# Optimization experiments

Measured on AMD Instinct MI355X. Metric: run time of the kernel, lower is better.

## Reference

```python
import jax, jax.numpy as jnp
import numpy as np

DK = 64  # embedding_size / h = 1024 / 16


def setup_inputs() -> dict:
    key = jax.random.key(0)
    k1, k2, k3 = jax.random.split(key, 3)
    S = 8192
    return {
        "q": jax.random.normal(k1, (S, DK), dtype=jnp.float32),
        "k": jax.random.normal(k2, (S, DK), dtype=jnp.float32),
        "v": jax.random.normal(k3, (S, DK), dtype=jnp.float32),
    }


def reference(q, k, v):
    # scores: [S, S]; NOTE: source scales by 1/dk (not 1/sqrt(dk)) — kept faithful.
    qk = jnp.matmul(q, k.T) * (1.0 / DK)
    S = qk.shape[0]
    # causal mask: position (i, j) allowed iff i >= j (0 added), else -inf
    i = jnp.arange(S)[:, None]
    j = jnp.arange(S)[None, :]
    qk = jnp.where(i >= j, qk, -jnp.inf)
    attn = jax.nn.softmax(qk, axis=-1)
    return jnp.matmul(attn, v)
```

## Files before the change

kernel.cpp:

```cpp
#include <hip/hip_runtime.h>
#include <hip/hip_bf16.h>

#define S_LEN 8192
#define DKD   64
#define BM    64
#define BN    64
#define PAD   8
#define LDK   (DKD + PAD)

#define CHUNK 1024
#define NC    (S_LEN / CHUNK)

#define WS_NEED ((size_t)2 * S_LEN * DKD * 2 + (size_t)NC * S_LEN * 4 + (size_t)NC * S_LEN * DKD * 2)

typedef __bf16 bf16x8 __attribute__((ext_vector_type(8)));
typedef float  f32x4  __attribute__((ext_vector_type(4)));
typedef unsigned short ushort8v __attribute__((ext_vector_type(8)));
typedef unsigned short ushort4v __attribute__((ext_vector_type(4)));

__device__ __forceinline__ unsigned short f2bf(float f) {
  union { float f; unsigned u; } v; v.f = f;
  unsigned u = v.u;
  return (unsigned short)((u + 0x7fffu + ((u >> 16) & 1u)) >> 16);
}
__device__ __forceinline__ float bf2f(unsigned short s) {
  union { unsigned u; float f; } v; v.u = ((unsigned)s) << 16;
  return v.f;
}
__device__ __forceinline__ unsigned pk2(float a, float b) {
  union { float f; unsigned u; } x, y; x.f = a; y.f = b;
  return ((x.u + 0x8000u) >> 16) | ((y.u + 0x8000u) & 0xffff0000u);
}
__device__ __forceinline__ bf16x8 q_frag8(const float* p, float sc) {
  float4 u = *(const float4*)p;
  float4 w = *(const float4*)(p + 4);
  union { ushort8v s; bf16x8 b; } r;
  r.s[0] = f2bf(u.x * sc); r.s[1] = f2bf(u.y * sc);
  r.s[2] = f2bf(u.z * sc); r.s[3] = f2bf(u.w * sc);
  r.s[4] = f2bf(w.x * sc); r.s[5] = f2bf(w.y * sc);
  r.s[6] = f2bf(w.z * sc); r.s[7] = f2bf(w.w * sc);
  return r.b;
}

__global__ __launch_bounds__(256) void precompute(const float* __restrict__ k,
                                                  const float* __restrict__ v,
                                                  unsigned short* __restrict__ Kb,
                                                  unsigned short* __restrict__ Vtb) {
  __shared__ unsigned short Ls[64][72];
  const int b = blockIdx.x, tid = threadIdx.x;
  if (blockIdx.y == 0) {
    size_t base = (size_t)b * 64 * DKD;
#pragma unroll
    for (int j = 0; j < 4; ++j) {
      int vi = tid + j * 256;
      float4 x = *(const float4*)(k + base + (size_t)vi * 4);
      ushort4v o = { f2bf(x.x), f2bf(x.y), f2bf(x.z), f2bf(x.w) };
      *(ushort4v*)(Kb + base + (size_t)vi * 4) = o;
    }
  } else {
#pragma unroll
    for (int j = 0; j < 4; ++j) {
      int vi = tid + j * 256;
      int row = vi >> 4, c4 = vi & 15;
      float4 x = *(const float4*)(v + ((size_t)(b * 64 + row)) * DKD + c4 * 4);
      Ls[row][c4 * 4 + 0] = f2bf(x.x);
      Ls[row][c4 * 4 + 1] = f2bf(x.y);
      Ls[row][c4 * 4 + 2] = f2bf(x.z);
      Ls[row][c4 * 4 + 3] = f2bf(x.w);
    }
    __syncthreads();
#pragma unroll
    for (int j = 0; j < 4; ++j) {
      int ci = tid + j * 256;
      int d = ci >> 4, c0 = ci & 15;
      ushort4v o = { Ls[c0][d], Ls[c0 + 16][d], Ls[c0 + 32][d], Ls[c0 + 48][d] };
      *(ushort4v*)(Vtb + (size_t)d * S_LEN + b * 64 + c0 * 4) = o;
    }
  }
}

__global__ __launch_bounds__(256) void attn_partial(const float* __restrict__ qg,
                                                    const unsigned short* __restrict__ Kb,
                                                    const unsigned short* __restrict__ Vtb,
                                                    unsigned short* __restrict__ Opart,
                                                    float* __restrict__ l_ws) {
  const int qt = blockIdx.x, cch = blockIdx.y;
  const int q0 = qt * BM, chunk0 = cch * CHUNK;
  if (chunk0 > q0) return;

  __shared__ __align__(16) unsigned short QP[BM][LDK];
  __shared__ __align__(16) unsigned short Ks[BN][LDK];
  __shared__ __align__(16) unsigned short Vts[DKD][LDK];

  const int tid = threadIdx.x, wave = tid >> 6, lane = tid & 63;
  const int col = lane & 15, quad = lane >> 4;
  const int n_kt = min(CHUNK / BN, ((q0 - chunk0) >> 6) + 1);

  const float* qp = qg + (size_t)(q0 + wave * 16 + col) * DKD;
  bf16x8 a0 = q_frag8(qp + quad * 8, 1.0f / 64.0f);
  bf16x8 a1 = q_frag8(qp + 32 + quad * 8, 1.0f / 64.0f);

#pragma unroll
  for (int j = 0; j < 2; ++j) {
    int vi = tid + j * 256, row = vi >> 3, ch = vi & 7;
    *(ushort8v*)&Ks[row][ch * 8]  = *(const ushort8v*)(Kb + ((size_t)(chunk0 + row)) * DKD + ch * 8);
    *(ushort8v*)&Vts[row][ch * 8] = *(const ushort8v*)(Vtb + (size_t)row * S_LEN + chunk0 + ch * 8);
  }
  __syncthreads();

  float lpart[4] = {0.0f, 0.0f, 0.0f, 0.0f};
  f32x4 Of[4];
#pragma unroll
  for (int i = 0; i < 4; ++i) Of[i] = f32x4{0.0f, 0.0f, 0.0f, 0.0f};

  ushort8v Kreg[2], Vreg[2];
  for (int it = 0; it < n_kt; ++it) {
    const int k0 = chunk0 + it * BN;
    const bool pf = (it + 1 < n_kt);

    if (pf) {
      const int k0n = k0 + BN;
#pragma unroll
      for (int j = 0; j < 2; ++j) {
        int vi = tid + j * 256, row = vi >> 3, ch = vi & 7;
        Kreg[j] = *(const ushort8v*)(Kb + ((size_t)(k0n + row)) * DKD + ch * 8);
        Vreg[j] = *(const ushort8v*)(Vtb + (size_t)row * S_LEN + k0n + ch * 8);
      }
    }

    f32x4 Sf[4];
#pragma unroll
    for (int t = 0; t < 4; ++t) {
      f32x4 acc = f32x4{0.0f, 0.0f, 0.0f, 0.0f};
      acc = __builtin_amdgcn_mfma_f32_16x16x32_bf16(a0, *(const bf16x8*)(&Ks[t * 16 + col][quad * 8]), acc, 0, 0, 0);
      acc = __builtin_amdgcn_mfma_f32_16x16x32_bf16(a1, *(const bf16x8*)(&Ks[t * 16 + col][32 + quad * 8]), acc, 0, 0, 0);
      Sf[t] = acc;
    }

    const int qb = q0 + wave * 16 + quad * 4;
#pragma unroll
    for (int t = 0; t < 4; ++t) {
      int kidx = k0 + t * 16 + col;
#pragma unroll
      for (int r = 0; r < 4; ++r) {
        float p = __expf(Sf[t][r]);
        p = (kidx <= qb + r) ? p : 0.0f;
        Sf[t][r] = p;
        lpart[r] += p;
      }
    }

#pragma unroll
    for (int r = 0; r < 4; ++r) {
      uint2 w2;
      w2.x = pk2(Sf[0][r], Sf[1][r]);
      w2.y = pk2(Sf[2][r], Sf[3][r]);
      *(uint2*)&QP[wave * 16 + quad * 4 + r][col * 4] = w2;
    }

    const unsigned short* prow = &QP[wave * 16 + col][0];
    bf16x8 pa0 = *(const bf16x8*)(prow + quad * 8);
    bf16x8 pa1 = *(const bf16x8*)(prow + 32 + quad * 8);
#pragma unroll
    for (int dt = 0; dt < 4; ++dt) {
      Of[dt] = __builtin_amdgcn_mfma_f32_16x16x32_bf16(pa0, *(const bf16x8*)(&Vts[dt * 16 + col][quad * 8]), Of[dt], 0, 0, 0);
      Of[dt] = __builtin_amdgcn_mfma_f32_16x16x32_bf16(pa1, *(const bf16x8*)(&Vts[dt * 16 + col][32 + quad * 8]), Of[dt], 0, 0, 0);
    }

    if (pf) {
      __syncthreads();
#pragma unroll
      for (int j = 0; j < 2; ++j) {
        int vi = tid + j * 256, row = vi >> 3, ch = vi & 7;
        *(ushort8v*)&Ks[row][ch * 8]  = Kreg[j];
        *(ushort8v*)&Vts[row][ch * 8] = Vreg[j];
      }
      __syncthreads();
    }
  }

#pragma unroll
  for (int off = 1; off <= 8; off <<= 1)
#pragma unroll
    for (int r = 0; r < 4; ++r)
      lpart[r] += __shfl_xor(lpart[r], off);

#pragma unroll
  for (int r = 0; r < 4; ++r) {
    int rowg = q0 + wave * 16 + quad * 4 + r;
    if (col == 0) l_ws[cch * S_LEN + rowg] = lpart[r];
    uint2 o2;
    o2.x = pk2(Of[0][r], Of[1][r]);
    o2.y = pk2(Of[2][r], Of[3][r]);
    *(uint2*)(Opart + ((size_t)cch * S_LEN + rowg) * DKD + col * 4) = o2;
  }
}

__global__ __launch_bounds__(256) void attn_merge(const unsigned short* __restrict__ Opart,
                                                  const float* __restrict__ l_ws,
                                                  float* __restrict__ out) {
  int idx = blockIdx.x * 256 + threadIdx.x;
  int row = idx >> 3, m = idx & 7;
  int nc = (row >> 10) + 1;

  float acc[8] = {0, 0, 0, 0, 0, 0, 0, 0};
  float L = 0.0f;
  for (int c = 0; c < nc; ++c) {
    L += l_ws[c * S_LEN + row];
    ushort8v o = *(const ushort8v*)(Opart + ((size_t)c * S_LEN + row) * DKD + m * 8);
#pragma unroll
    for (int j = 0; j < 8; ++j) acc[j] += bf2f(o[j]);
  }
  float inv = 1.0f / L;
#pragma unroll
  for (int j0 = 0; j0 < 4; ++j0) {
    float2 w = { acc[j0] * inv, acc[j0 + 4] * inv };
    *(float2*)(out + (size_t)row * DKD + 16 * j0 + 2 * m) = w;
  }
}

__global__ __launch_bounds__(128) void attn_fwd(const float* __restrict__ qg,
                                                const float* __restrict__ kg,
                                                const float* __restrict__ vg,
                                                float* __restrict__ out) {
  __shared__ __align__(16) unsigned short Qs[32][LDK];
  __shared__ __align__(16) unsigned short Ksh[BN][LDK];
  __shared__ __align__(16) unsigned short Vt[DKD][LDK];
  __shared__ __align__(16) unsigned short Ps[2][16][LDK];

  const int tid = threadIdx.x, wave = tid >> 6, lane = tid & 63;
  const int col = lane & 15, quad = lane >> 4;
  const int q0 = blockIdx.x * 32;

#pragma unroll
  for (int r = 0; r < 4; ++r) {
    int vi = tid + r * 128;
    int row = vi >> 4, c4 = vi & 15;
    if (row < 32) {
      float4 val = *(const float4*)(qg + (size_t)(q0 + row) * DKD + c4 * 4);
      Qs[row][c4 * 4 + 0] = f2bf(val.x);
      Qs[row][c4 * 4 + 1] = f2bf(val.y);
      Qs[row][c4 * 4 + 2] = f2bf(val.z);
      Qs[row][c4 * 4 + 3] = f2bf(val.w);
    }
  }

  float m_run[4], l_run[4];
  f32x4 Of[4];
#pragma unroll
  for (int i = 0; i < 4; ++i) {
    m_run[i] = -1e30f; l_run[i] = 0.0f;
    Of[i] = f32x4{0.0f, 0.0f, 0.0f, 0.0f};
  }

  const int n_tiles = (q0 + 32 - 1) / BN + 1;
  for (int it = 0; it < n_tiles; ++it) {
    __syncthreads();
    const int k0 = it * BN;
#pragma unroll
    for (int r = 0; r < 8; ++r) {
      int vi = tid + r * 128;
      int row = vi >> 4, c4 = vi & 15;
      float4 kv = *(const float4*)(kg + (size_t)(k0 + row) * DKD + c4 * 4);
      Ksh[row][c4 * 4 + 0] = f2bf(kv.x);
      Ksh[row][c4 * 4 + 1] = f2bf(kv.y);
      Ksh[row][c4 * 4 + 2] = f2bf(kv.z);
      Ksh[row][c4 * 4 + 3] = f2bf(kv.w);
      float4 vv = *(const float4*)(vg + (size_t)(k0 + row) * DKD + c4 * 4);
      Vt[c4 * 4 + 0][row] = f2bf(vv.x);
      Vt[c4 * 4 + 1][row] = f2bf(vv.y);
      Vt[c4 * 4 + 2][row] = f2bf(vv.z);
      Vt[c4 * 4 + 3][row] = f2bf(vv.w);
    }
    __syncthreads();

    f32x4 Sf[4];
    const unsigned short* qrow = &Qs[wave * 16 + col][0];
#pragma unroll
    for (int t = 0; t < 4; ++t) {
      f32x4 acc = f32x4{0.0f, 0.0f, 0.0f, 0.0f};
#pragma unroll
      for (int c = 0; c < 2; ++c) {
        bf16x8 a = *(const bf16x8*)(qrow + c * 32 + quad * 8);
        bf16x8 b = *(const bf16x8*)(&Ksh[t * 16 + col][c * 32 + quad * 8]);
        acc = __builtin_amdgcn_mfma_f32_16x16x32_bf16(a, b, acc, 0, 0, 0);
      }
      Sf[t] = acc;
    }

    const float scale = 1.0f / 64.0f;
    float rmax[4] = {-1e30f, -1e30f, -1e30f, -1e30f};
#pragma unroll
    for (int t = 0; t < 4; ++t) {
      int kidx = k0 + t * 16 + col;
#pragma unroll
      for (int r = 0; r < 4; ++r) {
        int qidx = q0 + wave * 16 + quad * 4 + r;
        float s = Sf[t][r] * scale;
        s = (kidx <= qidx) ? s : -1e30f;
        Sf[t][r] = s;
        rmax[r] = fmaxf(rmax[r], s);
      }
    }
#pragma unroll
    for (int off = 1; off <= 8; off <<= 1)
#pragma unroll
      for (int r = 0; r < 4; ++r)
        rmax[r] = fmaxf(rmax[r], __shfl_xor(rmax[r], off));

    float alpha[4], rsum[4];
#pragma unroll
    for (int r = 0; r < 4; ++r) {
      float mn = fmaxf(m_run[r], rmax[r]);
      alpha[r] = __expf(m_run[r] - mn);
      m_run[r] = mn;
      rsum[r] = 0.0f;
    }
#pragma unroll
    for (int t = 0; t < 4; ++t)
#pragma unroll
      for (int r = 0; r < 4; ++r) {
        float p = __expf(Sf[t][r] - m_run[r]);
        Sf[t][r] = p;
        rsum[r] += p;
      }
#pragma unroll
    for (int off = 1; off <= 8; off <<= 1)
#pragma unroll
      for (int r = 0; r < 4; ++r)
        rsum[r] += __shfl_xor(rsum[r], off);
#pragma unroll
    for (int r = 0; r < 4; ++r)
      l_run[r] = l_run[r] * alpha[r] + rsum[r];
#pragma unroll
    for (int dt = 0; dt < 4; ++dt)
#pragma unroll
      for (int r = 0; r < 4; ++r)
        Of[dt][r] *= alpha[r];

#pragma unroll
    for (int t = 0; t < 4; ++t)
#pragma unroll
      for (int r = 0; r < 4; ++r)
        Ps[wave][quad * 4 + r][t * 16 + col] = f2bf(Sf[t][r]);
    __syncthreads();

    const unsigned short* prow = &Ps[wave][col][0];
#pragma unroll
    for (int dt = 0; dt < 4; ++dt) {
#pragma unroll
      for (int c = 0; c < 2; ++c) {
        bf16x8 a = *(const bf16x8*)(prow + c * 32 + quad * 8);
        bf16x8 b = *(const bf16x8*)(&Vt[dt * 16 + col][c * 32 + quad * 8]);
        Of[dt] = __builtin_amdgcn_mfma_f32_16x16x32_bf16(a, b, Of[dt], 0, 0, 0);
      }
    }
  }

#pragma unroll
  for (int r = 0; r < 4; ++r) {
    float inv = 1.0f / l_run[r];
    int qrow_g = q0 + wave * 16 + quad * 4 + r;
#pragma unroll
    for (int dt = 0; dt < 4; ++dt)
      out[(size_t)qrow_g * DKD + dt * 16 + col] = Of[dt][r] * inv;
  }
}

extern "C" void kernel_launch(void* const* d_in, const int* in_sizes, int n_in,
                              void* d_out, int out_size, void* d_ws, size_t ws_size,
                              hipStream_t stream) {
  const float* q = (const float*)d_in[0];
  const float* k = (const float*)d_in[1];
  const float* v = (const float*)d_in[2];
  float* out = (float*)d_out;

  if (ws_size >= WS_NEED) {
    unsigned short* Kb  = (unsigned short*)d_ws;
    unsigned short* Vtb = Kb + (size_t)S_LEN * DKD;
    float* l_ws         = (float*)(Vtb + (size_t)S_LEN * DKD);
    unsigned short* Opart = (unsigned short*)(l_ws + (size_t)NC * S_LEN);

    hipLaunchKernelGGL(precompute, dim3(S_LEN / 64, 2), dim3(256), 0, stream, k, v, Kb, Vtb);
    hipLaunchKernelGGL(attn_partial, dim3(S_LEN / BM, NC), dim3(256), 0, stream,
                       q, Kb, Vtb, Opart, l_ws);
    hipLaunchKernelGGL(attn_merge, dim3(S_LEN * 8 / 256), dim3(256), 0, stream,
                       Opart, l_ws, out);
  } else {
    hipLaunchKernelGGL(attn_fwd, dim3(S_LEN / 32), dim3(128), 0, stream, q, k, v, out);
  }
}
```

Measured before the change: 100.1 us.

## Halve KV chunk size and double-buffer K/V prefetch two tiles ahead

Shrinks the split-KV chunk from 1024 to 512 keys, which doubles the number of partial blocks and the merge work but shortens the longest block's serial loop, improving load balance and parallelism. The partial kernel's loop is restructured into a ping-pong register double buffer that issues global loads two tiles ahead, so more memory latency is hidden behind the MFMA work. The merge kernel's chunk count is updated to match. In exchange the partial-output workspace traffic grows and register pressure rises from holding two prefetch sets.

```diff
diff --git a/kernel.cpp b/kernel.cpp
--- a/kernel.cpp
+++ b/kernel.cpp
@@ -8,7 +8,7 @@
 #define PAD   8
 #define LDK   (DKD + PAD)
 
-#define CHUNK 1024
+#define CHUNK 512
 #define NC    (S_LEN / CHUNK)
 
 #define WS_NEED ((size_t)2 * S_LEN * DKD * 2 + (size_t)NC * S_LEN * 4 + (size_t)NC * S_LEN * DKD * 2)
@@ -79,6 +79,48 @@
   }
 }
 
+__device__ __forceinline__ void tile_compute(
+    const unsigned short (*Ks)[LDK], const unsigned short (*Vts)[LDK],
+    unsigned short (*QP)[LDK],
+    bf16x8 a0, bf16x8 a1, int k0, int q0, int wave, int col, int quad,
+    float* lpart, f32x4* Of) {
+  f32x4 Sf[4];
+#pragma unroll
+  for (int t = 0; t < 4; ++t) {
+    f32x4 acc = f32x4{0.0f, 0.0f, 0.0f, 0.0f};
+    acc = __builtin_amdgcn_mfma_f32_16x16x32_bf16(a0, *(const bf16x8*)(&Ks[t * 16 + col][quad * 8]), acc, 0, 0, 0);
+    acc = __builtin_amdgcn_mfma_f32_16x16x32_bf16(a1, *(const bf16x8*)(&Ks[t * 16 + col][32 + quad * 8]), acc, 0, 0, 0);
+    Sf[t] = acc;
+  }
+  const int qb = q0 + wave * 16 + quad * 4;
+#pragma unroll
+  for (int t = 0; t < 4; ++t) {
+    int kidx = k0 + t * 16 + col;
+#pragma unroll
+    for (int r = 0; r < 4; ++r) {
+      float p = __expf(Sf[t][r]);
+      p = (kidx <= qb + r) ? p : 0.0f;
+      Sf[t][r] = p;
+      lpart[r] += p;
+    }
+  }
+#pragma unroll
+  for (int r = 0; r < 4; ++r) {
+    uint2 w2;
+    w2.x = pk2(Sf[0][r], Sf[1][r]);
+    w2.y = pk2(Sf[2][r], Sf[3][r]);
+    *(uint2*)&QP[wave * 16 + quad * 4 + r][col * 4] = w2;
+  }
+  const unsigned short* prow = &QP[wave * 16 + col][0];
+  bf16x8 pa0 = *(const bf16x8*)(prow + quad * 8);
+  bf16x8 pa1 = *(const bf16x8*)(prow + 32 + quad * 8);
+#pragma unroll
+  for (int dt = 0; dt < 4; ++dt) {
+    Of[dt] = __builtin_amdgcn_mfma_f32_16x16x32_bf16(pa0, *(const bf16x8*)(&Vts[dt * 16 + col][quad * 8]), Of[dt], 0, 0, 0);
+    Of[dt] = __builtin_amdgcn_mfma_f32_16x16x32_bf16(pa1, *(const bf16x8*)(&Vts[dt * 16 + col][32 + quad * 8]), Of[dt], 0, 0, 0);
+  }
+}
+
 __global__ __launch_bounds__(256) void attn_partial(const float* __restrict__ qg,
                                                     const unsigned short* __restrict__ Kb,
                                                     const unsigned short* __restrict__ Vtb,
@@ -96,88 +138,61 @@
   const int col = lane & 15, quad = lane >> 4;
   const int n_kt = min(CHUNK / BN, ((q0 - chunk0) >> 6) + 1);
 
+  const int srow0 = tid >> 3, sch0 = tid & 7;
+  const int srow1 = (tid + 256) >> 3, sch1 = tid & 7;
+  const unsigned short* kbase = Kb + (size_t)chunk0 * DKD;
+  const unsigned short* vbase = Vtb + chunk0;
+
   const float* qp = qg + (size_t)(q0 + wave * 16 + col) * DKD;
   bf16x8 a0 = q_frag8(qp + quad * 8, 1.0f / 64.0f);
   bf16x8 a1 = q_frag8(qp + 32 + quad * 8, 1.0f / 64.0f);
 
-#pragma unroll
-  for (int j = 0; j < 2; ++j) {
-    int vi = tid + j * 256, row = vi >> 3, ch = vi & 7;
-    *(ushort8v*)&Ks[row][ch * 8]  = *(const ushort8v*)(Kb + ((size_t)(chunk0 + row)) * DKD + ch * 8);
-    *(ushort8v*)&Vts[row][ch * 8] = *(const ushort8v*)(Vtb + (size_t)row * S_LEN + chunk0 + ch * 8);
-  }
-  __syncthreads();
-
   float lpart[4] = {0.0f, 0.0f, 0.0f, 0.0f};
   f32x4 Of[4];
 #pragma unroll
   for (int i = 0; i < 4; ++i) Of[i] = f32x4{0.0f, 0.0f, 0.0f, 0.0f};
 
-  ushort8v Kreg[2], Vreg[2];
-  for (int it = 0; it < n_kt; ++it) {
-    const int k0 = chunk0 + it * BN;
-    const bool pf = (it + 1 < n_kt);
-
-    if (pf) {
-      const int k0n = k0 + BN;
-#pragma unroll
-      for (int j = 0; j < 2; ++j) {
-        int vi = tid + j * 256, row = vi >> 3, ch = vi & 7;
-        Kreg[j] = *(const ushort8v*)(Kb + ((size_t)(k0n + row)) * DKD + ch * 8);
-        Vreg[j] = *(const ushort8v*)(Vtb + (size_t)row * S_LEN + k0n + ch * 8);
-      }
-    }
-
-    f32x4 Sf[4];
-#pragma unroll
-    for (int t = 0; t < 4; ++t) {
-      f32x4 acc = f32x4{0.0f, 0.0f, 0.0f, 0.0f};
-      acc = __builtin_amdgcn_mfma_f32_16x16x32_bf16(a0, *(const bf16x8*)(&Ks[t * 16 + col][quad * 8]), acc, 0, 0, 0);
-      acc = __builtin_amdgcn_mfma_f32_16x16x32_bf16(a1, *(const bf16x8*)(&Ks[t * 16 + col][32 + quad * 8]), acc, 0, 0, 0);
-      Sf[t] = acc;
-    }
-
-    const int qb = q0 + wave * 16 + quad * 4;
-#pragma unroll
-    for (int t = 0; t < 4; ++t) {
-      int kidx = k0 + t * 16 + col;
-#pragma unroll
-      for (int r = 0; r < 4; ++r) {
-        float p = __expf(Sf[t][r]);
-        p = (kidx <= qb + r) ? p : 0.0f;
-        Sf[t][r] = p;
-        lpart[r] += p;
-      }
-    }
-
-#pragma unroll
-    for (int r = 0; r < 4; ++r) {
-      uint2 w2;
-      w2.x = pk2(Sf[0][r], Sf[1][r]);
-      w2.y = pk2(Sf[2][r], Sf[3][r]);
-      *(uint2*)&QP[wave * 16 + quad * 4 + r][col * 4] = w2;
-    }
-
-    const unsigned short* prow = &QP[wave * 16 + col][0];
-    bf16x8 pa0 = *(const bf16x8*)(prow + quad * 8);
-    bf16x8 pa1 = *(const bf16x8*)(prow + 32 + quad * 8);
-#pragma unroll
-    for (int dt = 0; dt < 4; ++dt) {
-      Of[dt] = __builtin_amdgcn_mfma_f32_16x16x32_bf16(pa0, *(const bf16x8*)(&Vts[dt * 16 + col][quad * 8]), Of[dt], 0, 0, 0);
-      Of[dt] = __builtin_amdgcn_mfma_f32_16x16x32_bf16(pa1, *(const bf16x8*)(&Vts[dt * 16 + col][32 + quad * 8]), Of[dt], 0, 0, 0);
-    }
-
-    if (pf) {
-      __syncthreads();
-#pragma unroll
-      for (int j = 0; j < 2; ++j) {
-        int vi = tid + j * 256, row = vi >> 3, ch = vi & 7;
-        *(ushort8v*)&Ks[row][ch * 8]  = Kreg[j];
-        *(ushort8v*)&Vts[row][ch * 8] = Vreg[j];
-      }
-      __syncthreads();
-    }
-  }
+#define LOADT(Kd0, Kd1, Vd0, Vd1, toff)                                              \
+  do {                                                                               \
+    Kd0 = *(const ushort8v*)(kbase + ((size_t)((toff) + srow0)) * DKD + sch0 * 8);   \
+    Kd1 = *(const ushort8v*)(kbase + ((size_t)((toff) + srow1)) * DKD + sch1 * 8);   \
+    Vd0 = *(const ushort8v*)(vbase + (size_t)srow0 * S_LEN + (toff) + sch0 * 8);     \
+    Vd1 = *(const ushort8v*)(vbase + (size_t)srow1 * S_LEN + (toff) + sch1 * 8);     \
+  } while (0)
+#define STORET(Ks0, Ks1, Vs0, Vs1)                                                   \
+  do {                                                                               \
+    *(ushort8v*)&Ks[srow0][sch0 * 8]  = Ks0;                                         \
+    *(ushort8v*)&Ks[srow1][sch1 * 8]  = Ks1;                                         \
+    *(ushort8v*)&Vts[srow0][sch0 * 8] = Vs0;                                         \
+    *(ushort8v*)&Vts[srow1][sch1 * 8] = Vs1;                                         \
+  } while (0)
+
+  ushort8v Ka0, Ka1, Vaa0, Vaa1;
+  ushort8v Kb0, Kb1, Vbb0, Vbb1;
+
+  LOADT(Ka0, Ka1, Vaa0, Vaa1, 0);
+  STORET(Ka0, Ka1, Vaa0, Vaa1);
+  __syncthreads();
+  if (n_kt > 1) LOADT(Kb0, Kb1, Vbb0, Vbb1, BN);
+
+  int it = 0;
+  while (true) {
+    if (it + 2 < n_kt) LOADT(Ka0, Ka1, Vaa0, Vaa1, (it + 2) * BN);
+    tile_compute(Ks, Vts, QP, a0, a1, chunk0 + it * BN, q0, wave, col, quad, lpart, Of);
+    if (++it == n_kt) break;
+    __syncthreads();
+    STORET(Kb0, Kb1, Vbb0, Vbb1);
+    __syncthreads();
+
+    if (it + 2 < n_kt) LOADT(Kb0, Kb1, Vbb0, Vbb1, (it + 2) * BN);
+    tile_compute(Ks, Vts, QP, a0, a1, chunk0 + it * BN, q0, wave, col, quad, lpart, Of);
+    if (++it == n_kt) break;
+    __syncthreads();
+    STORET(Ka0, Ka1, Vaa0, Vaa1);
+    __syncthreads();
+  }
+#undef LOADT
+#undef STORET
 
 #pragma unroll
   for (int off = 1; off <= 8; off <<= 1)
@@ -201,7 +216,7 @@
                                                   float* __restrict__ out) {
   int idx = blockIdx.x * 256 + threadIdx.x;
   int row = idx >> 3, m = idx & 7;
-  int nc = (row >> 10) + 1;
+  int nc = (row >> 9) + 1;
 
   float acc[8] = {0, 0, 0, 0, 0, 0, 0, 0};
   float L = 0.0f;
@@ -253,7 +268,7 @@
     Of[i] = f32x4{0.0f, 0.0f, 0.0f, 0.0f};
   }
 
-  const int n_tiles = (q0 + 32 - 1) / BN + 1;
+  const int n_tiles = (q0 + 31) / BN + 1;
   for (int it = 0; it < n_tiles; ++it) {
     __syncthreads();
     const int k0 = it * BN;
```

After: 95.45 us. 4.7% less time.

## Drop LDS staging in split-K attention; feed MFMA directly from global with transposed S

Applied to the files above, without the earlier changes.

Computes S transposed (K as the A operand, Q as B) so that the exp'd probabilities already sit in registers in the layout the PV MFMA needs, removing the LDS round-trip for P. K and V fragments are now read straight from global/L2 instead of being staged through shared memory with prefetch and barriers. The V transpose in preprocessing is permuted to match the new P register layout. CHUNK is halved to 512, which doubles the number of split-K partitions and the merge work in exchange for more parallelism. The risk is higher global-load latency per MFMA, since there is no LDS reuse across the four waves.

```diff
diff --git a/kernel.cpp b/kernel.cpp
--- a/kernel.cpp
+++ b/kernel.cpp
@@ -8,7 +8,7 @@
 #define PAD   8
 #define LDK   (DKD + PAD)
 
-#define CHUNK 1024
+#define CHUNK 512
 #define NC    (S_LEN / CHUNK)
 
 #define WS_NEED ((size_t)2 * S_LEN * DKD * 2 + (size_t)NC * S_LEN * 4 + (size_t)NC * S_LEN * DKD * 2)
@@ -73,8 +73,10 @@
     for (int j = 0; j < 4; ++j) {
       int ci = tid + j * 256;
       int d = ci >> 4, c0 = ci & 15;
-      ushort4v o = { Ls[c0][d], Ls[c0 + 16][d], Ls[c0 + 32][d], Ls[c0 + 48][d] };
-      *(ushort4v*)(Vtb + (size_t)d * S_LEN + b * 64 + c0 * 4) = o;
+      int kl = c0 * 4;
+      int s0 = ((((kl & 7) >> 2) + 2 * (kl >> 5)) << 4) + (((kl >> 3) & 3) << 2);
+      ushort4v o = { Ls[s0][d], Ls[s0 + 1][d], Ls[s0 + 2][d], Ls[s0 + 3][d] };
+      *(ushort4v*)(Vtb + (size_t)d * S_LEN + b * 64 + kl) = o;
     }
   }
 }
@@ -88,107 +90,70 @@
   const int q0 = qt * BM, chunk0 = cch * CHUNK;
   if (chunk0 > q0) return;
 
-  __shared__ __align__(16) unsigned short QP[BM][LDK];
-  __shared__ __align__(16) unsigned short Ks[BN][LDK];
-  __shared__ __align__(16) unsigned short Vts[DKD][LDK];
-
   const int tid = threadIdx.x, wave = tid >> 6, lane = tid & 63;
   const int col = lane & 15, quad = lane >> 4;
   const int n_kt = min(CHUNK / BN, ((q0 - chunk0) >> 6) + 1);
 
-  const float* qp = qg + (size_t)(q0 + wave * 16 + col) * DKD;
-  bf16x8 a0 = q_frag8(qp + quad * 8, 1.0f / 64.0f);
-  bf16x8 a1 = q_frag8(qp + 32 + quad * 8, 1.0f / 64.0f);
-
-#pragma unroll
-  for (int j = 0; j < 2; ++j) {
-    int vi = tid + j * 256, row = vi >> 3, ch = vi & 7;
-    *(ushort8v*)&Ks[row][ch * 8]  = *(const ushort8v*)(Kb + ((size_t)(chunk0 + row)) * DKD + ch * 8);
-    *(ushort8v*)&Vts[row][ch * 8] = *(const ushort8v*)(Vtb + (size_t)row * S_LEN + chunk0 + ch * 8);
-  }
-  __syncthreads();
-
-  float lpart[4] = {0.0f, 0.0f, 0.0f, 0.0f};
+  const int qidx = q0 + wave * 16 + col;
+  const float* qp = qg + (size_t)qidx * DKD;
+  bf16x8 b0 = q_frag8(qp + quad * 8, 1.0f / 64.0f);
+  bf16x8 b1 = q_frag8(qp + 32 + quad * 8, 1.0f / 64.0f);
+
+  const unsigned short* kfb = Kb + ((size_t)chunk0 + col) * DKD + quad * 8;
+  const unsigned short* vfb = Vtb + (size_t)col * S_LEN + chunk0 + quad * 8;
+
+  float lsum = 0.0f;
   f32x4 Of[4];
 #pragma unroll
   for (int i = 0; i < 4; ++i) Of[i] = f32x4{0.0f, 0.0f, 0.0f, 0.0f};
 
-  ushort8v Kreg[2], Vreg[2];
   for (int it = 0; it < n_kt; ++it) {
     const int k0 = chunk0 + it * BN;
-    const bool pf = (it + 1 < n_kt);
-
-    if (pf) {
-      const int k0n = k0 + BN;
-#pragma unroll
-      for (int j = 0; j < 2; ++j) {
-        int vi = tid + j * 256, row = vi >> 3, ch = vi & 7;
-        Kreg[j] = *(const ushort8v*)(Kb + ((size_t)(k0n + row)) * DKD + ch * 8);
-        Vreg[j] = *(const ushort8v*)(Vtb + (size_t)row * S_LEN + k0n + ch * 8);
-      }
-    }
 
     f32x4 Sf[4];
 #pragma unroll
     for (int t = 0; t < 4; ++t) {
+      const unsigned short* kr = kfb + ((size_t)(it * BN + t * 16)) * DKD;
       f32x4 acc = f32x4{0.0f, 0.0f, 0.0f, 0.0f};
-      acc = __builtin_amdgcn_mfma_f32_16x16x32_bf16(a0, *(const bf16x8*)(&Ks[t * 16 + col][quad * 8]), acc, 0, 0, 0);
-      acc = __builtin_amdgcn_mfma_f32_16x16x32_bf16(a1, *(const bf16x8*)(&Ks[t * 16 + col][32 + quad * 8]), acc, 0, 0, 0);
+      acc = __builtin_amdgcn_mfma_f32_16x16x32_bf16(*(const bf16x8*)kr, b0, acc, 0, 0, 0);
+      acc = __builtin_amdgcn_mfma_f32_16x16x32_bf16(*(const bf16x8*)(kr + 32), b1, acc, 0, 0, 0);
       Sf[t] = acc;
     }
 
-    const int qb = q0 + wave * 16 + quad * 4;
 #pragma unroll
     for (int t = 0; t < 4; ++t) {
-      int kidx = k0 + t * 16 + col;
+      int kbase = k0 + t * 16 + quad * 4;
 #pragma unroll
       for (int r = 0; r < 4; ++r) {
         float p = __expf(Sf[t][r]);
-        p = (kidx <= qb + r) ? p : 0.0f;
+        p = (kbase + r <= qidx) ? p : 0.0f;
         Sf[t][r] = p;
-        lpart[r] += p;
-      }
-    }
-
-#pragma unroll
-    for (int r = 0; r < 4; ++r) {
-      uint2 w2;
-      w2.x = pk2(Sf[0][r], Sf[1][r]);
-      w2.y = pk2(Sf[2][r], Sf[3][r]);
-      *(uint2*)&QP[wave * 16 + quad * 4 + r][col * 4] = w2;
-    }
-
-    const unsigned short* prow = &QP[wave * 16 + col][0];
-    bf16x8 pa0 = *(const bf16x8*)(prow + quad * 8);
-    bf16x8 pa1 = *(const bf16x8*)(prow + 32 + quad * 8);
+        lsum += p;
+      }
+    }
+
+    union { unsigned u[4]; bf16x8 b; } pa0, pa1;
+    pa0.u[0] = pk2(Sf[0][0], Sf[0][1]); pa0.u[1] = pk2(Sf[0][2], Sf[0][3]);
+    pa0.u[2] = pk2(Sf[1][0], Sf[1][1]); pa0.u[3] = pk2(Sf[1][2], Sf[1][3]);
+    pa1.u[0] = pk2(Sf[2][0], Sf[2][1]); pa1.u[1] = pk2(Sf[2][2], Sf[2][3]);
+    pa1.u[2] = pk2(Sf[3][0], Sf[3][1]); pa1.u[3] = pk2(Sf[3][2], Sf[3][3]);
+
 #pragma unroll
     for (int dt = 0; dt < 4; ++dt) {
-      Of[dt] = __builtin_amdgcn_mfma_f32_16x16x32_bf16(pa0, *(const bf16x8*)(&Vts[dt * 16 + col][quad * 8]), Of[dt], 0, 0, 0);
-      Of[dt] = __builtin_amdgcn_mfma_f32_16x16x32_bf16(pa1, *(const bf16x8*)(&Vts[dt * 16 + col][32 + quad * 8]), Of[dt], 0, 0, 0);
-    }
-
-    if (pf) {
-      __syncthreads();
-#pragma unroll
-      for (int j = 0; j < 2; ++j) {
-        int vi = tid + j * 256, row = vi >> 3, ch = vi & 7;
-        *(ushort8v*)&Ks[row][ch * 8]  = Kreg[j];
-        *(ushort8v*)&Vts[row][ch * 8] = Vreg[j];
-      }
-      __syncthreads();
-    }
-  }
-
-#pragma unroll
-  for (int off = 1; off <= 8; off <<= 1)
-#pragma unroll
-    for (int r = 0; r < 4; ++r)
-      lpart[r] += __shfl_xor(lpart[r], off);
+      const unsigned short* vr = vfb + (size_t)(dt * 16) * S_LEN + it * BN;
+      Of[dt] = __builtin_amdgcn_mfma_f32_16x16x32_bf16(pa0.b, *(const bf16x8*)vr, Of[dt], 0, 0, 0);
+      Of[dt] = __builtin_amdgcn_mfma_f32_16x16x32_bf16(pa1.b, *(const bf16x8*)(vr + 32), Of[dt], 0, 0, 0);
+    }
+  }
+
+  lsum += __shfl_xor(lsum, 16);
+  lsum += __shfl_xor(lsum, 32);
+  if (lane < 16)
+    l_ws[cch * S_LEN + q0 + wave * 16 + lane] = lsum;
 
 #pragma unroll
   for (int r = 0; r < 4; ++r) {
     int rowg = q0 + wave * 16 + quad * 4 + r;
-    if (col == 0) l_ws[cch * S_LEN + rowg] = lpart[r];
     uint2 o2;
     o2.x = pk2(Of[0][r], Of[1][r]);
     o2.y = pk2(Of[2][r], Of[3][r]);
@@ -201,7 +166,7 @@
                                                   float* __restrict__ out) {
   int idx = blockIdx.x * 256 + threadIdx.x;
   int row = idx >> 3, m = idx & 7;
-  int nc = (row >> 10) + 1;
+  int nc = (row >> 9) + 1;
 
   float acc[8] = {0, 0, 0, 0, 0, 0, 0, 0};
   float L = 0.0f;
@@ -253,7 +218,7 @@
     Of[i] = f32x4{0.0f, 0.0f, 0.0f, 0.0f};
   }
 
-  const int n_tiles = (q0 + 32 - 1) / BN + 1;
+  const int n_tiles = (q0 + 31) / BN + 1;
   for (int it = 0; it < n_tiles; ++it) {
     __syncthreads();
     const int k0 = it * BN;
```

Measured after the change: 171.3 us. +71.1%, slower.
